# Performance work log

Measured on AMD Instinct MI355X. Metric: run time of the kernel, lower is better.

Reference implementation:

```python
import jax, jax.numpy as jnp
import numpy as np

H = 15  # hidden_size_
NUM_LAYERS = 4


def lstm_layer(x, Wih, Whh, bih, bhh):
    # x: [B, T, D] -> [B, T, H]; PyTorch gate order: i, f, g, o
    B = x.shape[0]
    h0 = jnp.zeros((B, H), x.dtype)
    c0 = jnp.zeros((B, H), x.dtype)
    b = (bih + bhh).astype(x.dtype)

    def step(carry, xt):
        h, c = carry
        g = xt @ Wih.T + h @ Whh.T + b  # [B, 4H]
        i, f, gg, o = jnp.split(g, 4, axis=-1)
        i = jax.nn.sigmoid(i)
        f = jax.nn.sigmoid(f)
        gg = jnp.tanh(gg)
        o = jax.nn.sigmoid(o)
        c = f * c + i * gg
        h = o * jnp.tanh(c)
        return (h, c), h

    _, ys = jax.lax.scan(step, (h0, c0), jnp.swapaxes(x, 0, 1))  # [T, B, H]
    return jnp.swapaxes(ys, 0, 1)


def setup_inputs() -> dict:
    key = jax.random.key(0)
    ks = jax.random.split(key, 8)
    B, T, D = 512, 2048, 64
    emb = jax.random.normal(ks[0], (B, T, D), dtype=jnp.float32)
    # pack_padded_sequence needs lengths sorted descending, min length 1
    lengths = jnp.sort(jax.random.randint(ks[1], (B,), 1, T + 1))[::-1]
    s = 0.1
    W_ih0 = jax.random.normal(ks[2], (4 * H, D), dtype=jnp.float32) * s
    W_ihr = jax.random.normal(ks[3], (NUM_LAYERS - 1, 4 * H, H), dtype=jnp.float32) * s
    W_hh = jax.random.normal(ks[4], (NUM_LAYERS, 4 * H, H), dtype=jnp.float32) * s
    b_ih = jax.random.normal(ks[5], (NUM_LAYERS, 4 * H), dtype=jnp.float32) * s
    b_hh = jax.random.normal(ks[6], (NUM_LAYERS, 4 * H), dtype=jnp.float32) * s
    return {"embeddings": emb, "lengths": lengths, "W_ih0": W_ih0,
            "W_ihr": W_ihr, "W_hh": W_hh, "b_ih": b_ih, "b_hh": b_hh}


def reference(embeddings, lengths, W_ih0, W_ihr, W_hh, b_ih, b_hh):
    # 4-layer LSTM (eval mode: inter-layer dropout is identity).
    # Running the full padded length is equivalent to packed processing for the
    # gathered outputs, since output at t < length depends only on steps <= t.
    x = lstm_layer(embeddings, W_ih0, W_hh[0], b_ih[0], b_hh[0])
    for l in range(NUM_LAYERS - 1):
        x = lstm_layer(x, W_ihr[l], W_hh[l + 1], b_ih[l + 1], b_hh[l + 1])
    # gather last valid timestep per sequence: out[b, lengths[b]-1, :]
    idx = jnp.broadcast_to((lengths - 1)[:, None, None], (x.shape[0], 1, x.shape[2]))
    return jnp.take_along_axis(x, idx, axis=1).squeeze(1)  # [B, H]
```

## Files before the change

kernel.cpp:

```cpp
#include <hip/hip_runtime.h>

#define HID 15
#define NG  60
#define DIM 64
#define T2  2048
#define NLAY 4
#define BSZ 512

__device__ __forceinline__ float bfr(float x) {
    unsigned u = __float_as_uint(x);
    u = (u + 0x7FFFu + ((u >> 16) & 1u)) & 0xFFFF0000u;
    return __uint_as_float(u);
}
#define CH(acc, a, b) acc = bfr(acc + bfr((a) * (b)))

__device__ __forceinline__ float tanh_np(float z) {
    const float e = __expf(-2.0f * z);
    return bfr((1.0f - e) / (1.0f + e));
}
__device__ __forceinline__ float sig_np(float z) {
    const float e   = bfr(__expf(-z));
    const float den = bfr(1.0f + e);
    return bfr(1.0f / den);
}
__device__ __forceinline__ float b2f(unsigned short b) {
    return __uint_as_float(((unsigned)b) << 16);
}

__global__ __launch_bounds__(256, 1)
void proj0(const float* __restrict__ emb,
           const int*   __restrict__ lengths,
           const float* __restrict__ Wih0,
           unsigned short* __restrict__ pa)
{
    const int wave = threadIdx.x >> 6;
    const int lane = threadIdx.x & 63;
    const int g    = (lane < NG) ? lane : (NG - 1);

    __shared__ __align__(16) float xrow[4][64];

    float wx[DIM];
    #pragma unroll
    for (int q = 0; q < 16; ++q) {
        float4 w = *(const float4*)(Wih0 + g*DIM + 4*q);
        wx[4*q+0] = bfr(w.x); wx[4*q+1] = bfr(w.y);
        wx[4*q+2] = bfr(w.z); wx[4*q+3] = bfr(w.w);
    }

    const int nrows = BSZ * T2;
    for (int r = blockIdx.x * 4 + wave; r < nrows; r += gridDim.x * 4) {
        const int b = r >> 11;
        const int t = r & (T2 - 1);
        if (t >= lengths[b]) continue;

        xrow[wave][lane] = bfr(emb[(size_t)r * DIM + lane]);
        const float4* xv = (const float4*)xrow[wave];
        float acc = 0.0f;
        #pragma unroll
        for (int q = 0; q < 16; ++q) {
            float4 v = xv[q];
            CH(acc, v.x, wx[4*q+0]);
            CH(acc, v.y, wx[4*q+1]);
            CH(acc, v.z, wx[4*q+2]);
            CH(acc, v.w, wx[4*q+3]);
        }
        if (lane < NG)
            pa[(size_t)r * NG + g] = (unsigned short)(__float_as_uint(acc) >> 16);
    }
}

__global__ __launch_bounds__(256, 1)
void lstm4_pipe(const int* __restrict__ lengths,
                const unsigned short* __restrict__ pa,
                const float* __restrict__ Wihr,
                const float* __restrict__ Whh,
                const float* __restrict__ bih,
                const float* __restrict__ bhh,
                float* __restrict__ out)
{
    const int s    = blockIdx.x;
    const int wave = threadIdx.x >> 6;
    const int lane = threadIdx.x & 63;
    const int g    = (lane < NG) ? lane : (NG - 1);

    __shared__ __align__(16) float h_lds[2][NLAY][16];

    float wr[16], wi[16];
    #pragma unroll
    for (int j = 0; j < HID; ++j) wr[j] = bfr(Whh[(wave*NG + g)*HID + j]);
    wr[15] = 0.0f;
    if (wave > 0) {
        #pragma unroll
        for (int j = 0; j < HID; ++j) wi[j] = bfr(Wihr[((wave-1)*NG + g)*HID + j]);
        wi[15] = 0.0f;
    } else {
        #pragma unroll
        for (int j = 0; j < 16; ++j) wi[j] = 0.0f;
    }
    const float bias_ = bfr(bfr(bih[wave*NG + g]) + bfr(bhh[wave*NG + g]));

    int len = lengths[s];
    len = len < 1 ? 1 : (len > T2 ? T2 : len);
    const unsigned short* pas = pa + (size_t)s * T2 * NG;

    float c_ = 0.0f;
    float hs[HID];
    #pragma unroll
    for (int j = 0; j < HID; ++j) hs[j] = 0.0f;

    unsigned short panb = 0;
    if (wave == 0) panb = pas[g];

    const bool tg = (lane >= 30 && lane < 45);

    for (int k = 0; k < len + NLAY - 1; ++k) {
        const int t = k - wave;
        if (t >= 0 && t < len) {
            float a_in = 0.0f, a_rec = 0.0f;
            float hv[16];

            if (wave > 0) {
                const float4* hp = (const float4*)h_lds[t & 1][wave - 1];
                *(float4*)&hv[0]  = hp[0]; *(float4*)&hv[4]  = hp[1];
                *(float4*)&hv[8]  = hp[2]; *(float4*)&hv[12] = hp[3];
            }

            #pragma unroll
            for (int j = 0; j < HID; ++j) CH(a_rec, hs[j], wr[j]);

            if (wave == 0) {
                a_in = b2f(panb);
                if (t + 1 < len) panb = pas[(size_t)(t + 1) * NG + g];
            } else {
                #pragma unroll
                for (int j = 0; j < HID; ++j) CH(a_in, hv[j], wi[j]);
            }

            const float z = bfr(bfr(a_in + a_rec) + bias_);
            const float a = tg ? tanh_np(z) : sig_np(z);

            const float fv = __shfl(a, (lane + 15) & 63);
            const float gv = __shfl(a, (lane + 30) & 63);
            const float ov = __shfl(a, (lane + 45) & 63);

            const float cn = bfr(bfr(fv * c_) + bfr(a * gv));
            c_ = cn;
            const float hn = bfr(ov * tanh_np(cn));

            #pragma unroll
            for (int j = 0; j < HID; ++j)
                hs[j] = __uint_as_float(__builtin_amdgcn_readlane(__float_as_uint(hn), j));

            if (lane < HID) h_lds[t & 1][wave][lane] = hn;
            if (wave == NLAY - 1 && t == len - 1 && lane < HID)
                out[s * HID + lane] = hn;
        }
        __syncthreads();
    }
}

__global__ __launch_bounds__(64, 1)
void lstm4_bf16np(const float* __restrict__ emb,
                  const int*   __restrict__ lengths,
                  const float* __restrict__ Wih0,
                  const float* __restrict__ Wihr,
                  const float* __restrict__ Whh,
                  const float* __restrict__ bih,
                  const float* __restrict__ bhh,
                  float* __restrict__ out)
{
    const int s    = blockIdx.x;
    const int lane = threadIdx.x;
    const int g    = (lane < NG) ? lane : (NG - 1);

    __shared__ __align__(16) float x_lds[DIM];
    __shared__ __align__(16) float h_lds[NLAY][16];

    float wx[DIM];
    #pragma unroll
    for (int q = 0; q < DIM/4; ++q) {
        float4 w = *(const float4*)(Wih0 + g*DIM + 4*q);
        wx[4*q+0] = bfr(w.x); wx[4*q+1] = bfr(w.y);
        wx[4*q+2] = bfr(w.z); wx[4*q+3] = bfr(w.w);
    }
    float wr[NLAY][16]; float wi[NLAY-1][16]; float bias[NLAY];
    #pragma unroll
    for (int l = 0; l < NLAY; ++l) {
        #pragma unroll
        for (int j = 0; j < HID; ++j) wr[l][j] = bfr(Whh[(l*NG + g)*HID + j]);
        wr[l][15] = 0.0f;
        bias[l] = bfr(bfr(bih[l*NG + g]) + bfr(bhh[l*NG + g]));
    }
    #pragma unroll
    for (int l = 0; l < NLAY-1; ++l) {
        #pragma unroll
        for (int j = 0; j < HID; ++j) wi[l][j] = bfr(Wihr[(l*NG + g)*HID + j]);
        wi[l][15] = 0.0f;
    }
    if (lane < 16) {
        #pragma unroll
        for (int l = 0; l < NLAY; ++l) h_lds[l][lane] = 0.0f;
    }
    float c[NLAY] = {0.0f, 0.0f, 0.0f, 0.0f};
    int len = lengths[s];
    len = len < 1 ? 1 : (len > T2 ? T2 : len);
    const float* xb = emb + (size_t)s * T2 * DIM;
    x_lds[lane] = bfr(xb[lane]);
    __syncthreads();
    const bool tg = (lane >= 30 && lane < 45);
    const float4* x4 = (const float4*)x_lds;
    float hout = 0.0f;
    for (int t = 0; t < len; ++t) {
        const int tn = (t + 1 < len) ? (t + 1) : t;
        const float xn = bfr(xb[(size_t)tn * DIM + lane]);
        #pragma unroll
        for (int l = 0; l < NLAY; ++l) {
            float a_in = 0.0f;
            if (l == 0) {
                #pragma unroll
                for (int q = 0; q < 16; ++q) {
                    float4 v = x4[q];
                    CH(a_in, v.x, wx[4*q+0]); CH(a_in, v.y, wx[4*q+1]);
                    CH(a_in, v.z, wx[4*q+2]); CH(a_in, v.w, wx[4*q+3]);
                }
            } else {
                const float4* hp = (const float4*)h_lds[l-1];
                float hv[16];
                *(float4*)&hv[0]  = hp[0]; *(float4*)&hv[4]  = hp[1];
                *(float4*)&hv[8]  = hp[2]; *(float4*)&hv[12] = hp[3];
                #pragma unroll
                for (int j = 0; j < HID; ++j) CH(a_in, hv[j], wi[l-1][j]);
            }
            float a_rec = 0.0f;
            {
                const float4* hc = (const float4*)h_lds[l];
                float hv[16];
                *(float4*)&hv[0]  = hc[0]; *(float4*)&hv[4]  = hc[1];
                *(float4*)&hv[8]  = hc[2]; *(float4*)&hv[12] = hc[3];
                #pragma unroll
                for (int j = 0; j < HID; ++j) CH(a_rec, hv[j], wr[l][j]);
            }
            const float z = bfr(bfr(a_in + a_rec) + bias[l]);
            const float a = tg ? tanh_np(z) : sig_np(z);
            const float fv = __shfl(a, (lane + 15) & 63);
            const float gv = __shfl(a, (lane + 30) & 63);
            const float ov = __shfl(a, (lane + 45) & 63);
            const float cn = bfr(bfr(fv * c[l]) + bfr(a * gv));
            c[l] = cn;
            const float hn = bfr(ov * tanh_np(cn));
            if (lane < HID) h_lds[l][lane] = hn;
            if (l == NLAY-1 && t == len-1) hout = hn;
        }
        x_lds[lane] = xn;
    }
    if (lane < HID) out[s * HID + lane] = hout;
}

extern "C" void kernel_launch(void* const* d_in, const int* in_sizes, int n_in,
                              void* d_out, int out_size, void* d_ws, size_t ws_size,
                              hipStream_t stream) {
    const float* emb     = (const float*)d_in[0];
    const int*   lengths = (const int*)  d_in[1];
    const float* Wih0    = (const float*)d_in[2];
    const float* Wihr    = (const float*)d_in[3];
    const float* Whh     = (const float*)d_in[4];
    const float* bih     = (const float*)d_in[5];
    const float* bhh     = (const float*)d_in[6];
    float* out = (float*)d_out;

    const size_t need = (size_t)BSZ * T2 * NG * sizeof(unsigned short);
    if (ws_size >= need) {
        unsigned short* pa = (unsigned short*)d_ws;
        proj0<<<2048, 256, 0, stream>>>(emb, lengths, Wih0, pa);
        lstm4_pipe<<<BSZ, 256, 0, stream>>>(lengths, pa, Wihr, Whh, bih, bhh, out);
    } else {
        lstm4_bf16np<<<BSZ, 64, 0, stream>>>(emb, lengths, Wih0, Wihr, Whh, bih, bhh, out);
    }
}
```

Baseline: 2.396 ms.

## Split input projection onto separate waves in pipelined LSTM kernel

Moves the inter-layer input projection (h_{l-1} · W_ih) for layers 1-3 onto three extra waves, so each recurrent wave only does its recurrent dot product and gate math. The block grows from 4 to 7 waves, and partial input sums pass through LDS, with two barriers per step instead of one. This shortens the serial per-step critical path of each layer wave, at the cost of an extra __syncthreads per timestep and more waves per block.

```diff
diff --git a/kernel.cpp b/kernel.cpp
--- a/kernel.cpp
+++ b/kernel.cpp
@@ -69,7 +69,7 @@
     }
 }
 
-__global__ __launch_bounds__(256, 1)
+__global__ __launch_bounds__(448, 1)
 void lstm4_pipe(const int* __restrict__ lengths,
                 const unsigned short* __restrict__ pa,
                 const float* __restrict__ Wihr,
@@ -84,78 +84,94 @@
     const int g    = (lane < NG) ? lane : (NG - 1);
 
     __shared__ __align__(16) float h_lds[2][NLAY][16];
-
-    float wr[16], wi[16];
-    #pragma unroll
-    for (int j = 0; j < HID; ++j) wr[j] = bfr(Whh[(wave*NG + g)*HID + j]);
-    wr[15] = 0.0f;
-    if (wave > 0) {
-        #pragma unroll
-        for (int j = 0; j < HID; ++j) wi[j] = bfr(Wihr[((wave-1)*NG + g)*HID + j]);
-        wi[15] = 0.0f;
-    } else {
-        #pragma unroll
-        for (int j = 0; j < 16; ++j) wi[j] = 0.0f;
-    }
-    const float bias_ = bfr(bfr(bih[wave*NG + g]) + bfr(bhh[wave*NG + g]));
+    __shared__ __align__(16) float a_in_lds[NLAY][64];
 
     int len = lengths[s];
     len = len < 1 ? 1 : (len > T2 ? T2 : len);
-    const unsigned short* pas = pa + (size_t)s * T2 * NG;
-
-    float c_ = 0.0f;
-    float hs[HID];
-    #pragma unroll
-    for (int j = 0; j < HID; ++j) hs[j] = 0.0f;
-
-    unsigned short panb = 0;
-    if (wave == 0) panb = pas[g];
 
     const bool tg = (lane >= 30 && lane < 45);
 
-    for (int k = 0; k < len + NLAY - 1; ++k) {
-        const int t = k - wave;
-        if (t >= 0 && t < len) {
-            float a_in = 0.0f, a_rec = 0.0f;
-            float hv[16];
-
-            if (wave > 0) {
-                const float4* hp = (const float4*)h_lds[t & 1][wave - 1];
+    if (wave < NLAY) {
+        const int l = wave;
+        float wr[16];
+        #pragma unroll
+        for (int j = 0; j < HID; ++j) wr[j] = bfr(Whh[(l*NG + g)*HID + j]);
+        wr[15] = 0.0f;
+        const float bias_ = bfr(bfr(bih[l*NG + g]) + bfr(bhh[l*NG + g]));
+
+        const unsigned short* pas = pa + (size_t)s * T2 * NG;
+
+        float c_ = 0.0f;
+        float hs[HID];
+        #pragma unroll
+        for (int j = 0; j < HID; ++j) hs[j] = 0.0f;
+
+        unsigned short panb = 0;
+        if (l == 0) panb = pas[g];
+
+        for (int k = 0; k < len + NLAY - 1; ++k) {
+            const int t = k - l;
+            const bool valid = (t >= 0) & (t < len);
+
+            float a_rec = 0.0f, a_in0 = 0.0f;
+            if (valid) {
+                #pragma unroll
+                for (int j = 0; j < HID; ++j) CH(a_rec, hs[j], wr[j]);
+                if (l == 0) {
+                    a_in0 = b2f(panb);
+                    if (t + 1 < len) panb = pas[(size_t)(t + 1) * NG + g];
+                }
+            }
+            __syncthreads();
+
+            if (valid) {
+                const float a_in = (l == 0) ? a_in0 : a_in_lds[l][g];
+                const float z = bfr(bfr(a_in + a_rec) + bias_);
+                const float a = tg ? tanh_np(z) : sig_np(z);
+
+                const float fv = __shfl(a, (lane + 15) & 63);
+                const float gv = __shfl(a, (lane + 30) & 63);
+                const float ov = __shfl(a, (lane + 45) & 63);
+
+                const float cn = bfr(bfr(fv * c_) + bfr(a * gv));
+                c_ = cn;
+                const float hn = bfr(ov * tanh_np(cn));
+
+                #pragma unroll
+                for (int j = 0; j < HID; ++j)
+                    hs[j] = __uint_as_float(__builtin_amdgcn_readlane(__float_as_uint(hn), j));
+
+                if (lane < HID) h_lds[t & 1][l][lane] = hn;
+                if (l == NLAY - 1 && t == len - 1 && lane < HID)
+                    out[s * HID + lane] = hn;
+            }
+            __syncthreads();
+        }
+    } else {
+        const int L = wave - 3;
+        float wi[16];
+        #pragma unroll
+        for (int j = 0; j < HID; ++j) wi[j] = bfr(Wihr[((L-1)*NG + g)*HID + j]);
+        wi[15] = 0.0f;
+
+        for (int k = 0; k < len + NLAY - 1; ++k) {
+            const int t = k - L;
+            const bool valid = (t >= 0) & (t < len);
+
+            if (valid) {
+                float hv[16];
+                const float4* hp = (const float4*)h_lds[t & 1][L - 1];
                 *(float4*)&hv[0]  = hp[0]; *(float4*)&hv[4]  = hp[1];
                 *(float4*)&hv[8]  = hp[2]; *(float4*)&hv[12] = hp[3];
-            }
-
-            #pragma unroll
-            for (int j = 0; j < HID; ++j) CH(a_rec, hs[j], wr[j]);
-
-            if (wave == 0) {
-                a_in = b2f(panb);
-                if (t + 1 < len) panb = pas[(size_t)(t + 1) * NG + g];
-            } else {
+
+                float a_in = 0.0f;
                 #pragma unroll
                 for (int j = 0; j < HID; ++j) CH(a_in, hv[j], wi[j]);
-            }
-
-            const float z = bfr(bfr(a_in + a_rec) + bias_);
-            const float a = tg ? tanh_np(z) : sig_np(z);
-
-            const float fv = __shfl(a, (lane + 15) & 63);
-            const float gv = __shfl(a, (lane + 30) & 63);
-            const float ov = __shfl(a, (lane + 45) & 63);
-
-            const float cn = bfr(bfr(fv * c_) + bfr(a * gv));
-            c_ = cn;
-            const float hn = bfr(ov * tanh_np(cn));
-
-            #pragma unroll
-            for (int j = 0; j < HID; ++j)
-                hs[j] = __uint_as_float(__builtin_amdgcn_readlane(__float_as_uint(hn), j));
-
-            if (lane < HID) h_lds[t & 1][wave][lane] = hn;
-            if (wave == NLAY - 1 && t == len - 1 && lane < HID)
-                out[s * HID + lane] = hn;
-        }
-        __syncthreads();
+                a_in_lds[L][lane] = a_in;
+            }
+            __syncthreads();
+            __syncthreads();
+        }
     }
 }
 
@@ -272,7 +288,7 @@
     if (ws_size >= need) {
         unsigned short* pa = (unsigned short*)d_ws;
         proj0<<<2048, 256, 0, stream>>>(emb, lengths, Wih0, pa);
-        lstm4_pipe<<<BSZ, 256, 0, stream>>>(lengths, pa, Wihr, Whh, bih, bhh, out);
+        lstm4_pipe<<<BSZ, 448, 0, stream>>>(lengths, pa, Wihr, Whh, bih, bhh, out);
     } else {
         lstm4_bf16np<<<BSZ, 64, 0, stream>>>(emb, lengths, Wih0, Wihr, Whh, bih, bhh, out);
     }
```

Result: slower. 2.571 ms (+7.3%).

## Interleave two sequences per block in pipelined LSTM and prefetch projection inputs

Applied to the files above, without the earlier changes.

The layer-pipelined LSTM kernel now processes two batch sequences per 256-thread block, interleaving their independent dependency chains to expose instruction-level parallelism and halve the block count. The input projection kernel prefetches the next embedding row into a register before computing the current one. This trades higher register pressure, and extra loads for padded rows, for better latency hiding.

```diff
diff --git a/kernel.cpp b/kernel.cpp
--- a/kernel.cpp
+++ b/kernel.cpp
@@ -47,113 +47,154 @@
         wx[4*q+2] = bfr(w.z); wx[4*q+3] = bfr(w.w);
     }
 
-    const int nrows = BSZ * T2;
-    for (int r = blockIdx.x * 4 + wave; r < nrows; r += gridDim.x * 4) {
+    const int nrows  = BSZ * T2;
+    const int stride = gridDim.x * 4;
+    const int r0     = blockIdx.x * 4 + wave;
+
+    float x_reg = 0.0f;
+    if (r0 < nrows) x_reg = emb[(size_t)r0 * DIM + lane];
+
+    for (int r = r0; r < nrows; r += stride) {
+        const int rn = r + stride;
+        float xnext = 0.0f;
+        if (rn < nrows) xnext = emb[(size_t)rn * DIM + lane];
+
+        xrow[wave][lane] = bfr(x_reg);
+
         const int b = r >> 11;
         const int t = r & (T2 - 1);
-        if (t >= lengths[b]) continue;
-
-        xrow[wave][lane] = bfr(emb[(size_t)r * DIM + lane]);
-        const float4* xv = (const float4*)xrow[wave];
-        float acc = 0.0f;
-        #pragma unroll
-        for (int q = 0; q < 16; ++q) {
-            float4 v = xv[q];
-            CH(acc, v.x, wx[4*q+0]);
-            CH(acc, v.y, wx[4*q+1]);
-            CH(acc, v.z, wx[4*q+2]);
-            CH(acc, v.w, wx[4*q+3]);
+        if (t < lengths[b]) {
+            const float4* xv = (const float4*)xrow[wave];
+            float acc = 0.0f;
+            #pragma unroll
+            for (int q = 0; q < 16; ++q) {
+                float4 v = xv[q];
+                CH(acc, v.x, wx[4*q+0]);
+                CH(acc, v.y, wx[4*q+1]);
+                CH(acc, v.z, wx[4*q+2]);
+                CH(acc, v.w, wx[4*q+3]);
+            }
+            if (lane < NG)
+                pa[(size_t)r * NG + g] = (unsigned short)(__float_as_uint(acc) >> 16);
         }
-        if (lane < NG)
-            pa[(size_t)r * NG + g] = (unsigned short)(__float_as_uint(acc) >> 16);
+        x_reg = xnext;
     }
 }
 
 __global__ __launch_bounds__(256, 1)
-void lstm4_pipe(const int* __restrict__ lengths,
-                const unsigned short* __restrict__ pa,
-                const float* __restrict__ Wihr,
-                const float* __restrict__ Whh,
-                const float* __restrict__ bih,
-                const float* __restrict__ bhh,
-                float* __restrict__ out)
+void lstm4_pipe2(const int* __restrict__ lengths,
+                 const unsigned short* __restrict__ pa,
+                 const float* __restrict__ Wihr,
+                 const float* __restrict__ Whh,
+                 const float* __restrict__ bih,
+                 const float* __restrict__ bhh,
+                 float* __restrict__ out)
 {
-    const int s    = blockIdx.x;
+    const int sA   = blockIdx.x * 2;
+    const int sB   = sA + 1;
     const int wave = threadIdx.x >> 6;
     const int lane = threadIdx.x & 63;
     const int g    = (lane < NG) ? lane : (NG - 1);
 
-    __shared__ __align__(16) float h_lds[2][NLAY][16];
-
+    __shared__ __align__(16) float h_lds[2][2][NLAY][16];
+
+    const int l = wave;
     float wr[16], wi[16];
     #pragma unroll
-    for (int j = 0; j < HID; ++j) wr[j] = bfr(Whh[(wave*NG + g)*HID + j]);
+    for (int j = 0; j < HID; ++j) wr[j] = bfr(Whh[(l*NG + g)*HID + j]);
     wr[15] = 0.0f;
-    if (wave > 0) {
-        #pragma unroll
-        for (int j = 0; j < HID; ++j) wi[j] = bfr(Wihr[((wave-1)*NG + g)*HID + j]);
+    if (l > 0) {
+        #pragma unroll
+        for (int j = 0; j < HID; ++j) wi[j] = bfr(Wihr[((l-1)*NG + g)*HID + j]);
         wi[15] = 0.0f;
     } else {
         #pragma unroll
         for (int j = 0; j < 16; ++j) wi[j] = 0.0f;
     }
-    const float bias_ = bfr(bfr(bih[wave*NG + g]) + bfr(bhh[wave*NG + g]));
-
-    int len = lengths[s];
-    len = len < 1 ? 1 : (len > T2 ? T2 : len);
-    const unsigned short* pas = pa + (size_t)s * T2 * NG;
-
-    float c_ = 0.0f;
-    float hs[HID];
-    #pragma unroll
-    for (int j = 0; j < HID; ++j) hs[j] = 0.0f;
-
-    unsigned short panb = 0;
-    if (wave == 0) panb = pas[g];
-
-    const bool tg = (lane >= 30 && lane < 45);
-
-    for (int k = 0; k < len + NLAY - 1; ++k) {
-        const int t = k - wave;
-        if (t >= 0 && t < len) {
-            float a_in = 0.0f, a_rec = 0.0f;
-            float hv[16];
-
-            if (wave > 0) {
-                const float4* hp = (const float4*)h_lds[t & 1][wave - 1];
-                *(float4*)&hv[0]  = hp[0]; *(float4*)&hv[4]  = hp[1];
-                *(float4*)&hv[8]  = hp[2]; *(float4*)&hv[12] = hp[3];
+    const float bias_ = bfr(bfr(bih[l*NG + g]) + bfr(bhh[l*NG + g]));
+
+    int lenA = lengths[sA]; lenA = lenA < 1 ? 1 : (lenA > T2 ? T2 : lenA);
+    int lenB = lengths[sB]; lenB = lenB < 1 ? 1 : (lenB > T2 ? T2 : lenB);
+    const unsigned short* pasA = pa + (size_t)sA * T2 * NG;
+    const unsigned short* pasB = pa + (size_t)sB * T2 * NG;
+
+    float cA = 0.0f, cB = 0.0f;
+    float hsA[HID], hsB[HID];
+    #pragma unroll
+    for (int j = 0; j < HID; ++j) { hsA[j] = 0.0f; hsB[j] = 0.0f; }
+
+    unsigned short panbA = 0, panbB = 0;
+    if (l == 0) { panbA = pasA[g]; panbB = pasB[g]; }
+
+    const bool tg  = (lane >= 30 && lane < 45);
+    const int lmax = (lenA > lenB) ? lenA : lenB;
+    const int nss  = lmax + NLAY - 1;
+
+    for (int k = 0; k < nss; ++k) {
+        const int t  = k - l;
+        const bool vA = (t >= 0) & (t < lenA);
+        const bool vB = (t >= 0) & (t < lenB);
+        if (vA | vB) {
+            float aiA = 0.0f, arA = 0.0f, aiB = 0.0f, arB = 0.0f;
+            float hvA[16], hvB[16];
+
+            if (l > 0) {
+                const float4* hpA = (const float4*)h_lds[0][t & 1][l - 1];
+                const float4* hpB = (const float4*)h_lds[1][t & 1][l - 1];
+                *(float4*)&hvA[0]  = hpA[0]; *(float4*)&hvA[4]  = hpA[1];
+                *(float4*)&hvA[8]  = hpA[2]; *(float4*)&hvA[12] = hpA[3];
+                *(float4*)&hvB[0]  = hpB[0]; *(float4*)&hvB[4]  = hpB[1];
+                *(float4*)&hvB[8]  = hpB[2]; *(float4*)&hvB[12] = hpB[3];
             }
 
             #pragma unroll
-            for (int j = 0; j < HID; ++j) CH(a_rec, hs[j], wr[j]);
-
-            if (wave == 0) {
-                a_in = b2f(panb);
-                if (t + 1 < len) panb = pas[(size_t)(t + 1) * NG + g];
+            for (int j = 0; j < HID; ++j) CH(arA, hsA[j], wr[j]);
+            #pragma unroll
+            for (int j = 0; j < HID; ++j) CH(arB, hsB[j], wr[j]);
+
+            if (l == 0) {
+                aiA = b2f(panbA);  aiB = b2f(panbB);
+                const int tnA = (t + 1 < lenA) ? (t + 1) : (lenA - 1);
+                const int tnB = (t + 1 < lenB) ? (t + 1) : (lenB - 1);
+                panbA = pasA[(size_t)tnA * NG + g];
+                panbB = pasB[(size_t)tnB * NG + g];
             } else {
                 #pragma unroll
-                for (int j = 0; j < HID; ++j) CH(a_in, hv[j], wi[j]);
-            }
-
-            const float z = bfr(bfr(a_in + a_rec) + bias_);
-            const float a = tg ? tanh_np(z) : sig_np(z);
-
-            const float fv = __shfl(a, (lane + 15) & 63);
-            const float gv = __shfl(a, (lane + 30) & 63);
-            const float ov = __shfl(a, (lane + 45) & 63);
-
-            const float cn = bfr(bfr(fv * c_) + bfr(a * gv));
-            c_ = cn;
-            const float hn = bfr(ov * tanh_np(cn));
+                for (int j = 0; j < HID; ++j) CH(aiA, hvA[j], wi[j]);
+                #pragma unroll
+                for (int j = 0; j < HID; ++j) CH(aiB, hvB[j], wi[j]);
+            }
+
+            const float zA = bfr(bfr(aiA + arA) + bias_);
+            const float zB = bfr(bfr(aiB + arB) + bias_);
+            const float aA = tg ? tanh_np(zA) : sig_np(zA);
+            const float aB = tg ? tanh_np(zB) : sig_np(zB);
+
+            const float fvA = __shfl(aA, (lane + 15) & 63);
+            const float gvA = __shfl(aA, (lane + 30) & 63);
+            const float ovA = __shfl(aA, (lane + 45) & 63);
+            const float fvB = __shfl(aB, (lane + 15) & 63);
+            const float gvB = __shfl(aB, (lane + 30) & 63);
+            const float ovB = __shfl(aB, (lane + 45) & 63);
+
+            const float cnA = bfr(bfr(fvA * cA) + bfr(aA * gvA));
+            const float cnB = bfr(bfr(fvB * cB) + bfr(aB * gvB));
+            cA = cnA; cB = cnB;
+            const float hnA = bfr(ovA * tanh_np(cnA));
+            const float hnB = bfr(ovB * tanh_np(cnB));
 
             #pragma unroll
-            for (int j = 0; j < HID; ++j)
-                hs[j] = __uint_as_float(__builtin_amdgcn_readlane(__float_as_uint(hn), j));
-
-            if (lane < HID) h_lds[t & 1][wave][lane] = hn;
-            if (wave == NLAY - 1 && t == len - 1 && lane < HID)
-                out[s * HID + lane] = hn;
+            for (int j = 0; j < HID; ++j) {
+                hsA[j] = __uint_as_float(__builtin_amdgcn_readlane(__float_as_uint(hnA), j));
+                hsB[j] = __uint_as_float(__builtin_amdgcn_readlane(__float_as_uint(hnB), j));
+            }
+
+            if (vA && lane < HID) h_lds[0][t & 1][l][lane] = hnA;
+            if (vB && lane < HID) h_lds[1][t & 1][l][lane] = hnB;
+            if (l == NLAY - 1 && lane < HID) {
+                if (t == lenA - 1) out[sA * HID + lane] = hnA;
+                if (t == lenB - 1) out[sB * HID + lane] = hnB;
+            }
         }
         __syncthreads();
     }
@@ -272,7 +313,7 @@
     if (ws_size >= need) {
         unsigned short* pa = (unsigned short*)d_ws;
         proj0<<<2048, 256, 0, stream>>>(emb, lengths, Wih0, pa);
-        lstm4_pipe<<<BSZ, 256, 0, stream>>>(lengths, pa, Wihr, Whh, bih, bhh, out);
+        lstm4_pipe2<<<BSZ/2, 256, 0, stream>>>(lengths, pa, Wihr, Whh, bih, bhh, out);
     } else {
         lstm4_bf16np<<<BSZ, 64, 0, stream>>>(emb, lengths, Wih0, Wihr, Whh, bih, bhh, out);
     }
```

After: 3.993 ms. +66.7%, slower.

## Batch LSTM pipeline steps into groups with LDS ring buffer and prefetch

Applied to the files above, without the earlier changes.

The 4-layer wavefront pipeline now advances in groups of 8 timesteps per barrier instead of one, passing hidden states between layers through a 16-deep LDS ring buffer. Layer 0 prefetches a group of projected inputs one group ahead instead of loading one step at a time. The projection kernel processes row pairs and software-prefetches the next embeddings. This cuts __syncthreads count and exposed load latency on the serial recurrence, at the cost of a longer pipeline fill and more registers.

```diff
diff --git a/kernel.cpp b/kernel.cpp
--- a/kernel.cpp
+++ b/kernel.cpp
@@ -6,6 +6,8 @@
 #define T2  2048
 #define NLAY 4
 #define BSZ 512
+#define DG  8
+#define RS  16
 
 __device__ __forceinline__ float bfr(float x) {
     unsigned u = __float_as_uint(x);
@@ -23,8 +25,8 @@
     const float den = bfr(1.0f + e);
     return bfr(1.0f / den);
 }
-__device__ __forceinline__ float b2f(unsigned short b) {
-    return __uint_as_float(((unsigned)b) << 16);
+__device__ __forceinline__ float b2f(unsigned b) {
+    return __uint_as_float(b << 16);
 }
 
 __global__ __launch_bounds__(256, 1)
@@ -37,7 +39,7 @@
     const int lane = threadIdx.x & 63;
     const int g    = (lane < NG) ? lane : (NG - 1);
 
-    __shared__ __align__(16) float xrow[4][64];
+    __shared__ __align__(16) float xrow[4][2][64];
 
     float wx[DIM];
     #pragma unroll
@@ -47,25 +49,50 @@
         wx[4*q+2] = bfr(w.z); wx[4*q+3] = bfr(w.w);
     }
 
-    const int nrows = BSZ * T2;
-    for (int r = blockIdx.x * 4 + wave; r < nrows; r += gridDim.x * 4) {
-        const int b = r >> 11;
-        const int t = r & (T2 - 1);
-        if (t >= lengths[b]) continue;
-
-        xrow[wave][lane] = bfr(emb[(size_t)r * DIM + lane]);
-        const float4* xv = (const float4*)xrow[wave];
-        float acc = 0.0f;
-        #pragma unroll
-        for (int q = 0; q < 16; ++q) {
-            float4 v = xv[q];
-            CH(acc, v.x, wx[4*q+0]);
-            CH(acc, v.y, wx[4*q+1]);
-            CH(acc, v.z, wx[4*q+2]);
-            CH(acc, v.w, wx[4*q+3]);
-        }
-        if (lane < NG)
-            pa[(size_t)r * NG + g] = (unsigned short)(__float_as_uint(acc) >> 16);
+    const int npairs = (BSZ * T2) / 2;
+    const int stride = gridDim.x * 4;
+    const int p0     = blockIdx.x * 4 + wave;
+
+    float xr0 = 0.0f, xr1 = 0.0f;
+    if (p0 < npairs) {
+        xr0 = emb[(size_t)(2*p0)     * DIM + lane];
+        xr1 = emb[(size_t)(2*p0 + 1) * DIM + lane];
+    }
+
+    for (int p = p0; p < npairs; p += stride) {
+        const int pn = p + stride;
+        float xn0 = 0.0f, xn1 = 0.0f;
+        if (pn < npairs) {
+            xn0 = emb[(size_t)(2*pn)     * DIM + lane];
+            xn1 = emb[(size_t)(2*pn + 1) * DIM + lane];
+        }
+
+        const int r   = 2 * p;
+        const int b   = r >> 11;
+        const int t   = r & (T2 - 1);
+        const int len = lengths[b];
+
+        if (t < len) {
+            xrow[wave][0][lane] = bfr(xr0);
+            xrow[wave][1][lane] = bfr(xr1);
+            const float4* xv0 = (const float4*)xrow[wave][0];
+            const float4* xv1 = (const float4*)xrow[wave][1];
+            float a0 = 0.0f, a1 = 0.0f;
+            #pragma unroll
+            for (int q = 0; q < 16; ++q) {
+                float4 u = xv0[q]; float4 v = xv1[q];
+                CH(a0, u.x, wx[4*q+0]); CH(a1, v.x, wx[4*q+0]);
+                CH(a0, u.y, wx[4*q+1]); CH(a1, v.y, wx[4*q+1]);
+                CH(a0, u.z, wx[4*q+2]); CH(a1, v.z, wx[4*q+2]);
+                CH(a0, u.w, wx[4*q+3]); CH(a1, v.w, wx[4*q+3]);
+            }
+            if (lane < NG) {
+                pa[(size_t)r * NG + g] = (unsigned short)(__float_as_uint(a0) >> 16);
+                if (t + 1 < len)
+                    pa[(size_t)(r + 1) * NG + g] = (unsigned short)(__float_as_uint(a1) >> 16);
+            }
+        }
+        xr0 = xn0; xr1 = xn1;
     }
 }
 
@@ -83,21 +110,22 @@
     const int lane = threadIdx.x & 63;
     const int g    = (lane < NG) ? lane : (NG - 1);
 
-    __shared__ __align__(16) float h_lds[2][NLAY][16];
-
+    __shared__ __align__(16) float ring[NLAY-1][RS][16];
+
+    const int l = wave;
     float wr[16], wi[16];
     #pragma unroll
-    for (int j = 0; j < HID; ++j) wr[j] = bfr(Whh[(wave*NG + g)*HID + j]);
+    for (int j = 0; j < HID; ++j) wr[j] = bfr(Whh[(l*NG + g)*HID + j]);
     wr[15] = 0.0f;
-    if (wave > 0) {
-        #pragma unroll
-        for (int j = 0; j < HID; ++j) wi[j] = bfr(Wihr[((wave-1)*NG + g)*HID + j]);
+    if (l > 0) {
+        #pragma unroll
+        for (int j = 0; j < HID; ++j) wi[j] = bfr(Wihr[((l-1)*NG + g)*HID + j]);
         wi[15] = 0.0f;
     } else {
         #pragma unroll
         for (int j = 0; j < 16; ++j) wi[j] = 0.0f;
     }
-    const float bias_ = bfr(bfr(bih[wave*NG + g]) + bfr(bhh[wave*NG + g]));
+    const float bias_ = bfr(bfr(bih[l*NG + g]) + bfr(bhh[l*NG + g]));
 
     int len = lengths[s];
     len = len < 1 ? 1 : (len > T2 ? T2 : len);
@@ -108,52 +136,77 @@
     #pragma unroll
     for (int j = 0; j < HID; ++j) hs[j] = 0.0f;
 
-    unsigned short panb = 0;
-    if (wave == 0) panb = pas[g];
+    unsigned pan_c[DG], pan_n[DG];
+    if (l == 0) {
+        #pragma unroll
+        for (int d = 0; d < DG; ++d) {
+            const int tt = (d < len) ? d : (len - 1);
+            pan_n[d] = pas[(size_t)tt * NG + g];
+        }
+    }
 
     const bool tg = (lane >= 30 && lane < 45);
-
-    for (int k = 0; k < len + NLAY - 1; ++k) {
-        const int t = k - wave;
-        if (t >= 0 && t < len) {
-            float a_in = 0.0f, a_rec = 0.0f;
-            float hv[16];
-
-            if (wave > 0) {
-                const float4* hp = (const float4*)h_lds[t & 1][wave - 1];
-                *(float4*)&hv[0]  = hp[0]; *(float4*)&hv[4]  = hp[1];
-                *(float4*)&hv[8]  = hp[2]; *(float4*)&hv[12] = hp[3];
+    const int ngrp = (len + DG - 1) / DG;
+    const int G    = ngrp + NLAY - 1;
+
+    for (int grp = 0; grp < G; ++grp) {
+        const int myg = grp - l;
+        if (myg >= 0 && myg < ngrp) {
+            const int t0 = myg * DG;
+
+            if (l == 0) {
+                #pragma unroll
+                for (int d = 0; d < DG; ++d) pan_c[d] = pan_n[d];
+                #pragma unroll
+                for (int d = 0; d < DG; ++d) {
+                    int tt = t0 + DG + d; tt = (tt < len) ? tt : (len - 1);
+                    pan_n[d] = pas[(size_t)tt * NG + g];
+                }
             }
 
             #pragma unroll
-            for (int j = 0; j < HID; ++j) CH(a_rec, hs[j], wr[j]);
-
-            if (wave == 0) {
-                a_in = b2f(panb);
-                if (t + 1 < len) panb = pas[(size_t)(t + 1) * NG + g];
-            } else {
-                #pragma unroll
-                for (int j = 0; j < HID; ++j) CH(a_in, hv[j], wi[j]);
-            }
-
-            const float z = bfr(bfr(a_in + a_rec) + bias_);
-            const float a = tg ? tanh_np(z) : sig_np(z);
-
-            const float fv = __shfl(a, (lane + 15) & 63);
-            const float gv = __shfl(a, (lane + 30) & 63);
-            const float ov = __shfl(a, (lane + 45) & 63);
-
-            const float cn = bfr(bfr(fv * c_) + bfr(a * gv));
-            c_ = cn;
-            const float hn = bfr(ov * tanh_np(cn));
-
-            #pragma unroll
-            for (int j = 0; j < HID; ++j)
-                hs[j] = __uint_as_float(__builtin_amdgcn_readlane(__float_as_uint(hn), j));
-
-            if (lane < HID) h_lds[t & 1][wave][lane] = hn;
-            if (wave == NLAY - 1 && t == len - 1 && lane < HID)
-                out[s * HID + lane] = hn;
+            for (int d = 0; d < DG; ++d) {
+                const int t = t0 + d;
+                if (t < len) {
+                    float a_in = 0.0f, a_rec = 0.0f;
+                    float hv[16];
+
+                    if (l > 0) {
+                        const float4* hp = (const float4*)ring[l-1][t & (RS-1)];
+                        *(float4*)&hv[0]  = hp[0]; *(float4*)&hv[4]  = hp[1];
+                        *(float4*)&hv[8]  = hp[2]; *(float4*)&hv[12] = hp[3];
+                    }
+
+                    #pragma unroll
+                    for (int j = 0; j < HID; ++j) CH(a_rec, hs[j], wr[j]);
+
+                    if (l == 0) {
+                        a_in = b2f(pan_c[d]);
+                    } else {
+                        #pragma unroll
+                        for (int j = 0; j < HID; ++j) CH(a_in, hv[j], wi[j]);
+                    }
+
+                    const float z = bfr(bfr(a_in + a_rec) + bias_);
+                    const float a = tg ? tanh_np(z) : sig_np(z);
+
+                    const float fv = __shfl(a, (lane + 15) & 63);
+                    const float gv = __shfl(a, (lane + 30) & 63);
+                    const float ov = __shfl(a, (lane + 45) & 63);
+
+                    const float cn = bfr(bfr(fv * c_) + bfr(a * gv));
+                    c_ = cn;
+                    const float hn = bfr(ov * tanh_np(cn));
+
+                    #pragma unroll
+                    for (int j = 0; j < HID; ++j)
+                        hs[j] = __uint_as_float(__builtin_amdgcn_readlane(__float_as_uint(hn), j));
+
+                    if (l < NLAY - 1 && lane < HID) ring[l][t & (RS-1)][lane] = hn;
+                    if (l == NLAY - 1 && t == len - 1 && lane < HID)
+                        out[s * HID + lane] = hn;
+                }
+            }
         }
         __syncthreads();
     }
```

Result: no change. 2.367 ms (-1.2%).
